# Kernel tuning notes

Measured on AMD Instinct MI355X. Metric: run time of the kernel, lower is better.

Reference implementation:

```python
import jax, jax.numpy as jnp
import numpy as np

B, M, N = 2, 256, 256
K, P, Q, D = 8, 512, 512, 64
R, Pp, Qp, Dp = 128, 512, 512, 64
TEMP = float(np.sqrt(Dp))  # softmax temperature = sqrt(D')


def _xavier(key, shape):
    # xavier_uniform over last two dims (fan_in, fan_out), matching torch init on (K, d, D)
    fan_in, fan_out = shape[-2], shape[-1]
    lim = float(np.sqrt(6.0 / (fan_in + fan_out)))
    return jax.random.uniform(key, shape, jnp.float32, -lim, lim)


def setup_inputs() -> dict:
    key = jax.random.key(0)
    ks = jax.random.split(key, 9)
    return {
        "z": jax.random.normal(ks[0], (B, M, N, R), jnp.float32),
        "y_q": jax.random.normal(ks[1], (B, N, Qp), jnp.float32),
        "x_k": jax.random.normal(ks[2], (B, M, Pp), jnp.float32),
        "Theta_x": _xavier(ks[3], (K, P, D)),
        "Theta_y": _xavier(ks[4], (K, Q, D)),
        "Lam_x": _xavier(ks[5], (K, Pp, Dp)),
        "Lam_y": _xavier(ks[6], (K, Qp, Dp)),
        "Lam_zx": _xavier(ks[7], (K, R, Dp)),
        "Lam_zy": _xavier(ks[8], (K, R, Dp)),
    }


def reference(z, y_q, x_k, Theta_x, Theta_y, Lam_x, Lam_y, Lam_zx, Lam_zy):
    # --- mixed attention scores ---
    xt = jnp.einsum('bmp,kpd->bkmd', x_k, Lam_x)          # [B,K,M,D']
    yt = jnp.einsum('bnq,kqd->bknd', y_q, Lam_y)          # [B,K,N,D']
    r = jnp.einsum('bkmd,bknd->bkmn', xt, yt)             # pairwise term
    zy = jnp.einsum('bmnr,krd->bkmnd', z, Lam_zy)         # [B,K,M,N,D'] (large)
    r = r + jnp.einsum('bkmnd,bkmd->bkmn', zy, xt)
    r = r + jnp.einsum('bknd,bmnr,krd->bkmn', yt, z, Lam_zx)
    # --- generalised convolution (mask=None, bias=False) ---
    a = jax.nn.softmax(r / TEMP, axis=-2)                 # softmax over M (column-wise)
    xv = jnp.einsum('bmp,kpd->bkmd', x_k, Theta_x)        # value projection
    y = jnp.einsum('bkmn,bkmd,kqd->bnq', a, xv, Theta_y)  # [B,N,Q]
    return y
```

## Files before the change

kernel.cpp:

```cpp
#include <hip/hip_runtime.h>
#include <hip/hip_bf16.h>

#define LOG2E_OVER_T 0.18033688011112042f

typedef __attribute__((ext_vector_type(8))) short short8;
typedef __attribute__((ext_vector_type(4))) float f32x4;
typedef unsigned short ushort_t;
typedef unsigned long long ull_t;

#define MFMA16(a, b, c) __builtin_amdgcn_mfma_f32_16x16x32_bf16(a, b, c, 0, 0, 0)

__device__ __forceinline__ ushort_t f2bf(float f) {
    union { float f; unsigned u; } v; v.f = f;
    unsigned r = (v.u + 0x7fffu + ((v.u >> 16) & 1u)) >> 16;
    return (ushort_t)r;
}

__device__ __forceinline__ void split8(const float4 a, const float4 b,
                                       short8& hi, short8& lo)
{
    union { float f[8]; unsigned u[8]; } Z;
    Z.f[0] = a.x; Z.f[1] = a.y; Z.f[2] = a.z; Z.f[3] = a.w;
    Z.f[4] = b.x; Z.f[5] = b.y; Z.f[6] = b.z; Z.f[7] = b.w;
    union { unsigned u[4]; short8 s; } H, L;
    #pragma unroll
    for (int i = 0; i < 4; i++) {
        const unsigned u0 = Z.u[2 * i], u1 = Z.u[2 * i + 1];
        H.u[i] = __builtin_amdgcn_perm(u1, u0, 0x07060302u);
        union { unsigned u; float f; } h0, h1;
        h0.u = u0 & 0xffff0000u; h1.u = u1 & 0xffff0000u;
        union { float f; unsigned u; } l0, l1;
        l0.f = Z.f[2 * i] - h0.f; l1.f = Z.f[2 * i + 1] - h1.f;
        L.u[i] = __builtin_amdgcn_perm(l1.u, l0.u, 0x07060302u);
    }
    hi = H.s; lo = L.s;
}

__device__ __forceinline__ void mfma_core64(
    const ushort_t* __restrict__ Ag, int lda,
    const ushort_t* __restrict__ Btg, int ldb,
    int ksteps, f32x4 acc[2][2])
{
    __shared__ __align__(16) ushort_t As[64 * 40];
    __shared__ __align__(16) ushort_t Bs[64 * 40];
    const int t = threadIdx.x;
    const int srow = t >> 2, skc = (t & 3) * 8;
    const int lane = t & 63, w = t >> 6;
    const int wr = w >> 1, wc = w & 1;
    const int fr = lane & 15, kg = lane >> 4;
    const int aoff = (wr * 32 + fr) * 40 + kg * 8;
    const int boff = (wc * 32 + fr) * 40 + kg * 8;
    const long arow = (long)srow * lda + skc;
    const long brow = (long)srow * ldb + skc;

    short8 ra = *(const short8*)(Ag + arow);
    short8 rb = *(const short8*)(Btg + brow);
    for (int kt = 0; kt < ksteps; kt++) {
        __syncthreads();
        *(short8*)&As[srow * 40 + skc] = ra;
        *(short8*)&Bs[srow * 40 + skc] = rb;
        __syncthreads();
        if (kt + 1 < ksteps) {
            ra = *(const short8*)(Ag + arow + (kt + 1) * 32);
            rb = *(const short8*)(Btg + brow + (kt + 1) * 32);
        }
        short8 a0 = *(const short8*)&As[aoff];
        short8 a1 = *(const short8*)&As[aoff + 16 * 40];
        short8 b0 = *(const short8*)&Bs[boff];
        short8 b1 = *(const short8*)&Bs[boff + 16 * 40];
        acc[0][0] = MFMA16(a0, b0, acc[0][0]);
        acc[0][1] = MFMA16(a0, b1, acc[0][1]);
        acc[1][0] = MFMA16(a1, b0, acc[1][0]);
        acc[1][1] = MFMA16(a1, b1, acc[1][1]);
    }
}

__device__ __forceinline__ void zero_acc(f32x4 acc[2][2]) {
    const f32x4 z4 = {0.f, 0.f, 0.f, 0.f};
    acc[0][0] = z4; acc[0][1] = z4; acc[1][0] = z4; acc[1][1] = z4;
}

__global__ __launch_bounds__(256)
void convert_kernel(const float* __restrict__ x_k, const float* __restrict__ y_q,
                    const float* __restrict__ Lam_x, const float* __restrict__ Theta_x,
                    const float* __restrict__ Lam_y, const float* __restrict__ Lam_zy,
                    const float* __restrict__ Lam_zx, const float* __restrict__ Theta_y,
                    ushort_t* __restrict__ xkb, ushort_t* __restrict__ yqb,
                    ushort_t* __restrict__ WxTb, ushort_t* __restrict__ WyTb,
                    ushort_t* __restrict__ Zyb, ushort_t* __restrict__ Zxb,
                    ushort_t* __restrict__ TyTb, float* __restrict__ ssum)
{
    int i = blockIdx.x * 256 + threadIdx.x;
    if (i < 262144) { xkb[i] = f2bf(x_k[i]); return; }
    i -= 262144;
    if (i < 262144) { yqb[i] = f2bf(y_q[i]); return; }
    i -= 262144;
    if (i < 524288) {
        const int k = i >> 16, rem = i & 65535, dc = rem >> 9, p = i & 511;
        const float v = (dc < 64) ? Lam_x[((long)k * 512 + p) * 64 + dc]
                                  : Theta_x[((long)k * 512 + p) * 64 + dc - 64];
        WxTb[i] = f2bf(v); return;
    }
    i -= 524288;
    if (i < 262144) {
        const int k = i >> 15, d = (i >> 9) & 63, p = i & 511;
        WyTb[i] = f2bf(Lam_y[((long)k * 512 + p) * 64 + d]); return;
    }
    i -= 262144;
    if (i < 65536) { Zyb[i] = f2bf(Lam_zy[i]); return; }
    i -= 65536;
    if (i < 65536) { Zxb[i] = f2bf(Lam_zx[i]); return; }
    i -= 65536;
    if (i < 262144) {
        const int q = i >> 9, kd = i & 511, k = kd >> 6, d = kd & 63;
        TyTb[i] = f2bf(Theta_y[((long)k * 512 + q) * 64 + d]); return;
    }
    i -= 262144;
    ssum[i] = 0.f;
}

__global__ __launch_bounds__(256)
void proj_kernel(const ushort_t* __restrict__ xkb, const ushort_t* __restrict__ yqb,
                 const ushort_t* __restrict__ WxTb, const ushort_t* __restrict__ WyTb,
                 ushort_t* __restrict__ xtb, ushort_t* __restrict__ ytb,
                 ushort_t* __restrict__ xvTb)
{
    const int side = blockIdx.z;
    const int bx = blockIdx.x, by = blockIdx.y;
    if (side == 1 && bx >= 8) return;
    f32x4 acc[2][2]; zero_acc(acc);
    const int t = threadIdx.x, lane = t & 63, w = t >> 6;
    const int wr = w >> 1, wc = w & 1, fr = lane & 15, kg = lane >> 4;

    if (side == 0) {
        mfma_core64(xkb + (long)(by * 64) * 512, 512,
                    WxTb + (long)(bx * 64) * 512, 512, 16, acc);
        const int k = bx >> 1, isxv = bx & 1;
        #pragma unroll
        for (int mi = 0; mi < 2; mi++)
        #pragma unroll
        for (int ni = 0; ni < 2; ni++) {
            const int grow0 = by * 64 + wr * 32 + mi * 16 + kg * 4;
            const int b = grow0 >> 8, m0 = grow0 & 255;
            const int d = wc * 32 + ni * 16 + fr;
            if (!isxv) {
                #pragma unroll
                for (int j = 0; j < 4; j++)
                    xtb[(((long)(b * 8 + k)) * 256 + m0 + j) * 64 + d] = f2bf(acc[mi][ni][j]);
            } else {
                ull_t pk = (ull_t)f2bf(acc[mi][ni][0])
                         | ((ull_t)f2bf(acc[mi][ni][1]) << 16)
                         | ((ull_t)f2bf(acc[mi][ni][2]) << 32)
                         | ((ull_t)f2bf(acc[mi][ni][3]) << 48);
                *(ull_t*)&xvTb[(((long)(b * 8 + k)) * 64 + d) * 256 + m0] = pk;
            }
        }
    } else {
        mfma_core64(yqb + (long)(by * 64) * 512, 512,
                    WyTb + (long)(bx * 64) * 512, 512, 16, acc);
        const int k = bx;
        #pragma unroll
        for (int mi = 0; mi < 2; mi++)
        #pragma unroll
        for (int ni = 0; ni < 2; ni++)
        #pragma unroll
        for (int j = 0; j < 4; j++) {
            const int grow = by * 64 + wr * 32 + mi * 16 + kg * 4 + j;
            const int b = grow >> 8, n = grow & 255;
            const int d = wc * 32 + ni * 16 + fr;
            ytb[(((long)(b * 8 + k)) * 256 + n) * 64 + d] = f2bf(acc[mi][ni][j]);
        }
    }
}

__global__ __launch_bounds__(256)
void step2_kernel(const ushort_t* __restrict__ xtb, const ushort_t* __restrict__ ytb,
                  const ushort_t* __restrict__ Zyb, const ushort_t* __restrict__ Zxb,
                  ushort_t* __restrict__ wzyb, ushort_t* __restrict__ wzxb)
{
    const int bz = blockIdx.x;
    const int which = bz >> 7, idx = bz & 127;
    const int bk = idx >> 3, tile = idx & 7, mt = tile >> 1, nt = tile & 1;
    const int k = bk & 7, b = bk >> 3;
    const ushort_t* Ag  = (which ? ytb : xtb) + ((long)bk * 256 + mt * 64) * 64;
    const ushort_t* Btg = (which ? Zxb : Zyb) + ((long)k * 128 + nt * 64) * 64;
    ushort_t* C = which ? wzxb : wzyb;
    f32x4 acc[2][2]; zero_acc(acc);
    mfma_core64(Ag, 64, Btg, 64, 2, acc);
    const int t = threadIdx.x, lane = t & 63, w = t >> 6;
    const int wr = w >> 1, wc = w & 1, fr = lane & 15, kg = lane >> 4;
    #pragma unroll
    for (int mi = 0; mi < 2; mi++)
    #pragma unroll
    for (int ni = 0; ni < 2; ni++)
    #pragma unroll
    for (int j = 0; j < 4; j++) {
        const int m_glob = mt * 64 + wr * 32 + mi * 16 + kg * 4 + j;
        const int r_glob = nt * 64 + wc * 32 + ni * 16 + fr;
        C[(((long)b * 256 + m_glob) * 8 + k) * 128 + r_glob] = f2bf(acc[mi][ni][j]);
    }
}

__global__ __launch_bounds__(128)
void fused_score(const float* __restrict__ z,
                 const ushort_t* __restrict__ xtb, const ushort_t* __restrict__ ytb,
                 const ushort_t* __restrict__ wzyb, const ushort_t* __restrict__ wzxb,
                 ushort_t* __restrict__ Et, float* __restrict__ ssum)
{
    const int nt = blockIdx.x, mt = blockIdx.y, b = blockIdx.z;
    const int nbase = nt * 16, m0 = mt * 8;
    __shared__ float sc[2][8][8][17];

    const int tid = threadIdx.x;
    const int lane = tid & 63, w = tid >> 6;
    const int fr = lane & 15, kg = lane >> 4;
    const int f8 = fr & 7;
    const int rh = w * 64;

    if (w == 0) {
        #pragma unroll 2
        for (int k = 0; k < 8; k++) {
            const long kb = (long)(b * 8 + k) * 256;
            short8 a0 = *(const short8*)(ytb + (kb + nbase + fr) * 64 + kg * 8);
            short8 b0 = *(const short8*)(xtb + (kb + m0 + f8) * 64 + kg * 8);
            short8 a1 = *(const short8*)(ytb + (kb + nbase + fr) * 64 + 32 + kg * 8);
            short8 b1 = *(const short8*)(xtb + (kb + m0 + f8) * 64 + 32 + kg * 8);
            f32x4 acc = {0.f, 0.f, 0.f, 0.f};
            acc = MFMA16(a0, b0, acc);
            acc = MFMA16(a1, b1, acc);
            if (fr < 8) {
                #pragma unroll
                for (int j = 0; j < 4; j++)
                    sc[0][fr][k][kg * 4 + j] = acc[j];
            }
        }
    }

    #pragma unroll 2
    for (int m = 0; m < 8; m++) {
        const float* zp = z + (((long)b * 256 + m0 + m) * 256 + nbase + fr) * 128 + rh + kg * 8;
        const ushort_t* wp = wzyb + (((long)b * 256 + m0 + m) * 8 + f8) * 128 + rh + kg * 8;
        const float4 z00 = *(const float4*)(zp);
        const float4 z01 = *(const float4*)(zp + 4);
        const float4 z10 = *(const float4*)(zp + 32);
        const float4 z11 = *(const float4*)(zp + 36);
        const short8 w0 = *(const short8*)(wp);
        const short8 w1 = *(const short8*)(wp + 32);
        short8 h0, l0, h1, l1;
        split8(z00, z01, h0, l0);
        split8(z10, z11, h1, l1);
        f32x4 acc = {0.f, 0.f, 0.f, 0.f};
        acc = MFMA16(h0, w0, acc);
        acc = MFMA16(h1, w1, acc);
        acc = MFMA16(l0, w0, acc);
        acc = MFMA16(l1, w1, acc);
        if (fr < 8) {
            if (w == 0) {
                #pragma unroll
                for (int j = 0; j < 4; j++)
                    sc[0][m][fr][kg * 4 + j] += acc[j];
            } else {
                #pragma unroll
                for (int j = 0; j < 4; j++)
                    sc[1][m][fr][kg * 4 + j] = acc[j];
            }
        }
    }

    #pragma unroll 2
    for (int n = 0; n < 16; n++) {
        const float* zp = z + (((long)b * 256 + m0 + f8) * 256 + nbase + n) * 128 + rh + kg * 8;
        const ushort_t* wp = wzxb + (((long)b * 256 + nbase + n) * 8 + f8) * 128 + rh + kg * 8;
        const float4 z00 = *(const float4*)(zp);
        const float4 z01 = *(const float4*)(zp + 4);
        const float4 z10 = *(const float4*)(zp + 32);
        const float4 z11 = *(const float4*)(zp + 36);
        const short8 w0 = *(const short8*)(wp);
        const short8 w1 = *(const short8*)(wp + 32);
        short8 h0, l0, h1, l1;
        split8(z00, z01, h0, l0);
        split8(z10, z11, h1, l1);
        f32x4 acc = {0.f, 0.f, 0.f, 0.f};
        acc = MFMA16(h0, w0, acc);
        acc = MFMA16(h1, w1, acc);
        acc = MFMA16(l0, w0, acc);
        acc = MFMA16(l1, w1, acc);
        if (fr < 8 && kg < 2) {
            #pragma unroll
            for (int j = 0; j < 4; j++)
                sc[w][kg * 4 + j][fr][n] += acc[j];
        }
    }
    __syncthreads();

    {
        const int k = tid >> 4, n = tid & 15;
        float s8 = 0.f;
        ushort_t eb[8];
        #pragma unroll
        for (int m = 0; m < 8; m++) {
            const float e = exp2f((sc[0][m][k][n] + sc[1][m][k][n]) * LOG2E_OVER_T);
            eb[m] = f2bf(e);
            s8 += e;
        }
        *(short8*)(Et + (((long)b * 8 + k) * 256 + nbase + n) * 256 + m0) = *(short8*)eb;
        atomicAdd(&ssum[(b * 8 + k) * 256 + nbase + n], s8);
    }
}

__global__ __launch_bounds__(256)
void ogemm_kernel(const ushort_t* __restrict__ Et, const ushort_t* __restrict__ xvTb,
                  const float* __restrict__ ssum, ushort_t* __restrict__ o2b)
{
    const int mt = blockIdx.x, bk = blockIdx.y;
    f32x4 acc[2][2]; zero_acc(acc);
    mfma_core64(Et + ((long)bk * 256 + mt * 64) * 256, 256,
                xvTb + (long)bk * 64 * 256, 256, 8, acc);
    const int t = threadIdx.x, lane = t & 63, w = t >> 6;
    const int wr = w >> 1, wc = w & 1, fr = lane & 15, kg = lane >> 4;
    const int b = bk >> 3, k = bk & 7;
    #pragma unroll
    for (int mi = 0; mi < 2; mi++)
    #pragma unroll
    for (int j = 0; j < 4; j++) {
        const int n = mt * 64 + wr * 32 + mi * 16 + kg * 4 + j;
        const float inv = 1.0f / ssum[bk * 256 + n];
        #pragma unroll
        for (int ni = 0; ni < 2; ni++) {
            const int d = wc * 32 + ni * 16 + fr;
            o2b[((long)b * 256 + n) * 512 + k * 64 + d] = f2bf(acc[mi][ni][j] * inv);
        }
    }
}

__global__ __launch_bounds__(256)
void ygemm_kernel(const ushort_t* __restrict__ o2b, const ushort_t* __restrict__ TyTb,
                  float* __restrict__ out)
{
    const int qt = blockIdx.x, mt = blockIdx.y, b = blockIdx.z;
    f32x4 acc[2][2]; zero_acc(acc);
    mfma_core64(o2b + ((long)b * 256 + mt * 64) * 512, 512,
                TyTb + (long)qt * 64 * 512, 512, 16, acc);
    const int t = threadIdx.x, lane = t & 63, w = t >> 6;
    const int wr = w >> 1, wc = w & 1, fr = lane & 15, kg = lane >> 4;
    #pragma unroll
    for (int mi = 0; mi < 2; mi++)
    #pragma unroll
    for (int ni = 0; ni < 2; ni++)
    #pragma unroll
    for (int j = 0; j < 4; j++) {
        const int n = mt * 64 + wr * 32 + mi * 16 + kg * 4 + j;
        const int q = qt * 64 + wc * 32 + ni * 16 + fr;
        out[((long)b * 256 + n) * 512 + q] = acc[mi][ni][j];
    }
}

extern "C" void kernel_launch(void* const* d_in, const int* in_sizes, int n_in,
                              void* d_out, int out_size, void* d_ws, size_t ws_size,
                              hipStream_t stream)
{
    const float* z       = (const float*)d_in[0];
    const float* y_q     = (const float*)d_in[1];
    const float* x_k     = (const float*)d_in[2];
    const float* Theta_x = (const float*)d_in[3];
    const float* Theta_y = (const float*)d_in[4];
    const float* Lam_x   = (const float*)d_in[5];
    const float* Lam_y   = (const float*)d_in[6];
    const float* Lam_zx  = (const float*)d_in[7];
    const float* Lam_zy  = (const float*)d_in[8];
    float* out = (float*)d_out;

    ushort_t* U = (ushort_t*)d_ws;
    ushort_t* xkb  = U;
    ushort_t* yqb  = U + 262144;
    ushort_t* WxTb = U + 524288;
    ushort_t* WyTb = U + 1048576;
    ushort_t* Zyb  = U + 1310720;
    ushort_t* Zxb  = U + 1376256;
    ushort_t* TyTb = U + 1441792;
    ushort_t* xtb  = U + 1703936;
    ushort_t* ytb  = U + 1966080;
    ushort_t* xvTb = U + 2228224;
    ushort_t* wzyb = U + 2490368;
    ushort_t* wzxb = U + 3014656;
    ushort_t* Et   = U + 3538944;
    ushort_t* o2b  = U + 4587520;
    float*    ssum = (float*)(U + 4849664);

    convert_kernel<<<6672, 256, 0, stream>>>(x_k, y_q, Lam_x, Theta_x, Lam_y,
        Lam_zy, Lam_zx, Theta_y, xkb, yqb, WxTb, WyTb, Zyb, Zxb, TyTb, ssum);

    proj_kernel<<<dim3(16, 8, 2), 256, 0, stream>>>(xkb, yqb, WxTb, WyTb,
        xtb, ytb, xvTb);

    step2_kernel<<<256, 256, 0, stream>>>(xtb, ytb, Zyb, Zxb, wzyb, wzxb);

    fused_score<<<dim3(16, 32, 2), 128, 0, stream>>>(z, xtb, ytb, wzyb, wzxb,
        Et, ssum);

    ogemm_kernel<<<dim3(4, 16), 256, 0, stream>>>(Et, xvTb, ssum, o2b);

    ygemm_kernel<<<dim3(8, 4, 2), 256, 0, stream>>>(o2b, TyTb, out);
}
```

Baseline: 71.26 us.

## Move pairwise score GEMM to step2 and widen fused_score to four waves

```diff
diff --git a/kernel.cpp b/kernel.cpp
--- a/kernel.cpp
+++ b/kernel.cpp
@@ -176,130 +176,141 @@
 __global__ __launch_bounds__(256)
 void step2_kernel(const ushort_t* __restrict__ xtb, const ushort_t* __restrict__ ytb,
                   const ushort_t* __restrict__ Zyb, const ushort_t* __restrict__ Zxb,
-                  ushort_t* __restrict__ wzyb, ushort_t* __restrict__ wzxb)
+                  ushort_t* __restrict__ wzyb, ushort_t* __restrict__ wzxb,
+                  float* __restrict__ t1)
 {
     const int bz = blockIdx.x;
-    const int which = bz >> 7, idx = bz & 127;
-    const int bk = idx >> 3, tile = idx & 7, mt = tile >> 1, nt = tile & 1;
-    const int k = bk & 7, b = bk >> 3;
-    const ushort_t* Ag  = (which ? ytb : xtb) + ((long)bk * 256 + mt * 64) * 64;
-    const ushort_t* Btg = (which ? Zxb : Zyb) + ((long)k * 128 + nt * 64) * 64;
-    ushort_t* C = which ? wzxb : wzyb;
-    f32x4 acc[2][2]; zero_acc(acc);
-    mfma_core64(Ag, 64, Btg, 64, 2, acc);
     const int t = threadIdx.x, lane = t & 63, w = t >> 6;
     const int wr = w >> 1, wc = w & 1, fr = lane & 15, kg = lane >> 4;
-    #pragma unroll
-    for (int mi = 0; mi < 2; mi++)
-    #pragma unroll
-    for (int ni = 0; ni < 2; ni++)
-    #pragma unroll
-    for (int j = 0; j < 4; j++) {
-        const int m_glob = mt * 64 + wr * 32 + mi * 16 + kg * 4 + j;
-        const int r_glob = nt * 64 + wc * 32 + ni * 16 + fr;
-        C[(((long)b * 256 + m_glob) * 8 + k) * 128 + r_glob] = f2bf(acc[mi][ni][j]);
-    }
-}
-
-__global__ __launch_bounds__(128)
+
+    if (bz < 256) {
+        const int which = bz >> 7, idx = bz & 127;
+        const int bk = idx >> 3, tile = idx & 7, mt = tile >> 1, nt = tile & 1;
+        const int k = bk & 7, b = bk >> 3;
+        const ushort_t* Ag  = (which ? ytb : xtb) + ((long)bk * 256 + mt * 64) * 64;
+        const ushort_t* Btg = (which ? Zxb : Zyb) + ((long)k * 128 + nt * 64) * 64;
+        ushort_t* C = which ? wzxb : wzyb;
+        f32x4 acc[2][2]; zero_acc(acc);
+        mfma_core64(Ag, 64, Btg, 64, 2, acc);
+        #pragma unroll
+        for (int mi = 0; mi < 2; mi++)
+        #pragma unroll
+        for (int ni = 0; ni < 2; ni++)
+        #pragma unroll
+        for (int j = 0; j < 4; j++) {
+            const int m_glob = mt * 64 + wr * 32 + mi * 16 + kg * 4 + j;
+            const int r_glob = nt * 64 + wc * 32 + ni * 16 + fr;
+            C[(((long)b * 256 + m_glob) * 8 + k) * 128 + r_glob] = f2bf(acc[mi][ni][j]);
+        }
+    } else {
+        const int idx = bz - 256;
+        const int bk = idx >> 4, tile = idx & 15, nt2 = tile >> 2, mt2 = tile & 3;
+        f32x4 acc[2][2]; zero_acc(acc);
+        mfma_core64(ytb + ((long)bk * 256 + nt2 * 64) * 64, 64,
+                    xtb + ((long)bk * 256 + mt2 * 64) * 64, 64, 2, acc);
+        #pragma unroll
+        for (int mi = 0; mi < 2; mi++)
+        #pragma unroll
+        for (int ni = 0; ni < 2; ni++)
+        #pragma unroll
+        for (int j = 0; j < 4; j++) {
+            const int n_glob = nt2 * 64 + wr * 32 + mi * 16 + kg * 4 + j;
+            const int m_glob = mt2 * 64 + wc * 32 + ni * 16 + fr;
+            t1[((long)bk * 256 + n_glob) * 256 + m_glob] = acc[mi][ni][j];
+        }
+    }
+}
+
+__global__ __launch_bounds__(256)
 void fused_score(const float* __restrict__ z,
-                 const ushort_t* __restrict__ xtb, const ushort_t* __restrict__ ytb,
                  const ushort_t* __restrict__ wzyb, const ushort_t* __restrict__ wzxb,
-                 ushort_t* __restrict__ Et, float* __restrict__ ssum)
+                 const float* __restrict__ t1, ushort_t* __restrict__ Et,
+                 float* __restrict__ ssum)
 {
     const int nt = blockIdx.x, mt = blockIdx.y, b = blockIdx.z;
     const int nbase = nt * 16, m0 = mt * 8;
-    __shared__ float sc[2][8][8][17];
+    __shared__ float sc[4][8][8][17];
 
     const int tid = threadIdx.x;
     const int lane = tid & 63, w = tid >> 6;
     const int fr = lane & 15, kg = lane >> 4;
     const int f8 = fr & 7;
-    const int rh = w * 64;
-
-    if (w == 0) {
-        #pragma unroll 2
-        for (int k = 0; k < 8; k++) {
-            const long kb = (long)(b * 8 + k) * 256;
-            short8 a0 = *(const short8*)(ytb + (kb + nbase + fr) * 64 + kg * 8);
-            short8 b0 = *(const short8*)(xtb + (kb + m0 + f8) * 64 + kg * 8);
-            short8 a1 = *(const short8*)(ytb + (kb + nbase + fr) * 64 + 32 + kg * 8);
-            short8 b1 = *(const short8*)(xtb + (kb + m0 + f8) * 64 + 32 + kg * 8);
+    const int rh = w * 32;
+
+    {
+        const float* zp = z + (((long)b * 256 + m0) * 256 + nbase + fr) * 128 + rh + kg * 8;
+        const ushort_t* wp = wzyb + (((long)b * 256 + m0) * 8 + f8) * 128 + rh + kg * 8;
+        float4 za = *(const float4*)(zp);
+        float4 zb = *(const float4*)(zp + 4);
+        short8 wa = *(const short8*)(wp);
+        float4 zc = *(const float4*)(zp + 32768);
+        float4 zd = *(const float4*)(zp + 32768 + 4);
+        short8 wb = *(const short8*)(wp + 1024);
+        #pragma unroll
+        for (int m = 0; m < 8; m++) {
+            const int mnx = (m + 2 < 8) ? m + 2 : m;
+            float4 ze = *(const float4*)(zp + mnx * 32768);
+            float4 zf = *(const float4*)(zp + mnx * 32768 + 4);
+            short8 wc = *(const short8*)(wp + mnx * 1024);
+            short8 hi, lo;
+            split8(za, zb, hi, lo);
             f32x4 acc = {0.f, 0.f, 0.f, 0.f};
-            acc = MFMA16(a0, b0, acc);
-            acc = MFMA16(a1, b1, acc);
+            acc = MFMA16(hi, wa, acc);
+            acc = MFMA16(lo, wa, acc);
             if (fr < 8) {
                 #pragma unroll
                 for (int j = 0; j < 4; j++)
-                    sc[0][fr][k][kg * 4 + j] = acc[j];
+                    sc[w][m][fr][kg * 4 + j] = acc[j];
             }
-        }
-    }
-
-    #pragma unroll 2
-    for (int m = 0; m < 8; m++) {
-        const float* zp = z + (((long)b * 256 + m0 + m) * 256 + nbase + fr) * 128 + rh + kg * 8;
-        const ushort_t* wp = wzyb + (((long)b * 256 + m0 + m) * 8 + f8) * 128 + rh + kg * 8;
-        const float4 z00 = *(const float4*)(zp);
-        const float4 z01 = *(const float4*)(zp + 4);
-        const float4 z10 = *(const float4*)(zp + 32);
-        const float4 z11 = *(const float4*)(zp + 36);
-        const short8 w0 = *(const short8*)(wp);
-        const short8 w1 = *(const short8*)(wp + 32);
-        short8 h0, l0, h1, l1;
-        split8(z00, z01, h0, l0);
-        split8(z10, z11, h1, l1);
-        f32x4 acc = {0.f, 0.f, 0.f, 0.f};
-        acc = MFMA16(h0, w0, acc);
-        acc = MFMA16(h1, w1, acc);
-        acc = MFMA16(l0, w0, acc);
-        acc = MFMA16(l1, w1, acc);
-        if (fr < 8) {
-            if (w == 0) {
+            za = zc; zb = zd; wa = wb;
+            zc = ze; zd = zf; wb = wc;
+        }
+    }
+
+    {
+        const float* zp = z + (((long)b * 256 + m0 + f8) * 256 + nbase) * 128 + rh + kg * 8;
+        const ushort_t* wp = wzxb + (((long)b * 256 + nbase) * 8 + f8) * 128 + rh + kg * 8;
+        float4 za = *(const float4*)(zp);
+        float4 zb = *(const float4*)(zp + 4);
+        short8 wa = *(const short8*)(wp);
+        float4 zc = *(const float4*)(zp + 128);
+        float4 zd = *(const float4*)(zp + 128 + 4);
+        short8 wb = *(const short8*)(wp + 1024);
+        #pragma unroll
+        for (int n = 0; n < 16; n++) {
+            const int nnx = (n + 2 < 16) ? n + 2 : n;
+            float4 ze = *(const float4*)(zp + nnx * 128);
+            float4 zf = *(const float4*)(zp + nnx * 128 + 4);
+            short8 wc = *(const short8*)(wp + nnx * 1024);
+            short8 hi, lo;
+            split8(za, zb, hi, lo);
+            f32x4 acc = {0.f, 0.f, 0.f, 0.f};
+            acc = MFMA16(hi, wa, acc);
+            acc = MFMA16(lo, wa, acc);
+            if (fr < 8 && kg < 2) {
                 #pragma unroll
                 for (int j = 0; j < 4; j++)
-                    sc[0][m][fr][kg * 4 + j] += acc[j];
-            } else {
-                #pragma unroll
-                for (int j = 0; j < 4; j++)
-                    sc[1][m][fr][kg * 4 + j] = acc[j];
+                    sc[w][kg * 4 + j][fr][n] += acc[j];
             }
-        }
-    }
-
-    #pragma unroll 2
-    for (int n = 0; n < 16; n++) {
-        const float* zp = z + (((long)b * 256 + m0 + f8) * 256 + nbase + n) * 128 + rh + kg * 8;
-        const ushort_t* wp = wzxb + (((long)b * 256 + nbase + n) * 8 + f8) * 128 + rh + kg * 8;
-        const float4 z00 = *(const float4*)(zp);
-        const float4 z01 = *(const float4*)(zp + 4);
-        const float4 z10 = *(const float4*)(zp + 32);
-        const float4 z11 = *(const float4*)(zp + 36);
-        const short8 w0 = *(const short8*)(wp);
-        const short8 w1 = *(const short8*)(wp + 32);
-        short8 h0, l0, h1, l1;
-        split8(z00, z01, h0, l0);
-        split8(z10, z11, h1, l1);
-        f32x4 acc = {0.f, 0.f, 0.f, 0.f};
-        acc = MFMA16(h0, w0, acc);
-        acc = MFMA16(h1, w1, acc);
-        acc = MFMA16(l0, w0, acc);
-        acc = MFMA16(l1, w1, acc);
-        if (fr < 8 && kg < 2) {
-            #pragma unroll
-            for (int j = 0; j < 4; j++)
-                sc[w][kg * 4 + j][fr][n] += acc[j];
+            za = zc; zb = zd; wa = wb;
+            zc = ze; zd = zf; wb = wc;
         }
     }
     __syncthreads();
 
-    {
+    if (tid < 128) {
         const int k = tid >> 4, n = tid & 15;
+        const float* tp = t1 + (((long)b * 8 + k) * 256 + nbase + n) * 256 + m0;
+        const float4 t0 = *(const float4*)(tp);
+        const float4 t4 = *(const float4*)(tp + 4);
+        const float tv[8] = {t0.x, t0.y, t0.z, t0.w, t4.x, t4.y, t4.z, t4.w};
         float s8 = 0.f;
         ushort_t eb[8];
         #pragma unroll
         for (int m = 0; m < 8; m++) {
-            const float e = exp2f((sc[0][m][k][n] + sc[1][m][k][n]) * LOG2E_OVER_T);
+            const float s = sc[0][m][k][n] + sc[1][m][k][n]
+                          + sc[2][m][k][n] + sc[3][m][k][n] + tv[m];
+            const float e = exp2f(s * LOG2E_OVER_T);
             eb[m] = f2bf(e);
             s8 += e;
         }
@@ -386,6 +397,7 @@
     ushort_t* Et   = U + 3538944;
     ushort_t* o2b  = U + 4587520;
     float*    ssum = (float*)(U + 4849664);
+    float*    t1   = (float*)(U + 4857856);
 
     convert_kernel<<<6672, 256, 0, stream>>>(x_k, y_q, Lam_x, Theta_x, Lam_y,
         Lam_zy, Lam_zx, Theta_y, xkb, yqb, WxTb, WyTb, Zyb, Zxb, TyTb, ssum);
@@ -393,9 +405,9 @@
     proj_kernel<<<dim3(16, 8, 2), 256, 0, stream>>>(xkb, yqb, WxTb, WyTb,
         xtb, ytb, xvTb);
 
-    step2_kernel<<<256, 256, 0, stream>>>(xtb, ytb, Zyb, Zxb, wzyb, wzxb);
-
-    fused_score<<<dim3(16, 32, 2), 128, 0, stream>>>(z, xtb, ytb, wzyb, wzxb,
+    step2_kernel<<<512, 256, 0, stream>>>(xtb, ytb, Zyb, Zxb, wzyb, wzxb, t1);
+
+    fused_score<<<dim3(16, 32, 2), 256, 0, stream>>>(z, wzyb, wzxb, t1,
         Et, ssum);
 
     ogemm_kernel<<<dim3(4, 16), 256, 0, stream>>>(Et, xvTb, ssum, o2b);
```

Result: no change. 70.00 us (-1.8%).
